# Performance work log

Measured on AMD Instinct MI355X. Metric: run time of the kernel, lower is better.

Reference implementation:

```python
import jax, jax.numpy as jnp
import numpy as np

TEMPERATURE = 8.0  # sqrt(d_k), d_k = 64

def setup_inputs() -> dict:
    key = jax.random.key(0)
    kq, kk, kv, km = jax.random.split(key, 4)
    B, H, S, D = 4, 16, 1024, 64
    q = jax.random.normal(kq, (B, H, S, D), dtype=jnp.float32)
    k = jax.random.normal(kk, (B, H, S, D), dtype=jnp.float32)
    v = jax.random.normal(kv, (B, H, S, D), dtype=jnp.float32)
    mask = jax.random.randint(km, (B, 1, S, S), 0, 2, dtype=jnp.int32)
    return {"q": q, "k": k, "v": v, "mask": mask}

def reference(q, k, v, mask):
    # scores: [B,H,S,S]
    attn = jnp.einsum("bhqd,bhkd->bhqk", q, k) / TEMPERATURE
    attn = jnp.where(mask == 0, jnp.float32(-1e9), attn)
    attn = jax.nn.softmax(attn, axis=-1)
    output = jnp.einsum("bhqk,bhkd->bhqd", attn, v)
    return (output, attn)
```

## Files before the change

kernel.cpp:

```cpp
#include <hip/hip_runtime.h>
#include <hip/hip_bf16.h>

#define S_LEN 1024
#define DH 64
#define QB 64
#define KT 64
#define NKT 16
#define LDP 72

typedef __attribute__((ext_vector_type(8))) short bf16x8;
typedef __attribute__((ext_vector_type(4))) float f32x4;
typedef unsigned long long u64;

__device__ __forceinline__ unsigned short f2bf(float f) {
  unsigned u = __float_as_uint(f);
  u = u + 0x7FFFu + ((u >> 16) & 1u);
  return (unsigned short)(u >> 16);
}
__device__ __forceinline__ float bf2f(unsigned short s) {
  return __uint_as_float((unsigned)s << 16);
}
__device__ __forceinline__ unsigned pk2(float a, float b) {
  __hip_bfloat162 h = __float22bfloat162_rn(float2{a, b});
  return *reinterpret_cast<unsigned*>(&h);
}

__global__ __launch_bounds__(256)
void maskpack_kernel(const int* __restrict__ mask, u64* __restrict__ bits) {
  int w    = blockIdx.x * 4 + (threadIdx.x >> 6);
  int lane = threadIdx.x & 63;
  int m = mask[(size_t)w * 64 + lane];
  u64 word = __ballot(m != 0);
  if (lane == 0) bits[w] = word;
}

__global__ __launch_bounds__(256, 4)
void sdpa_kernel(const float* __restrict__ qg, const float* __restrict__ kg,
                 const float* __restrict__ vg, const u64* __restrict__ bitsg,
                 float* __restrict__ outg, float* __restrict__ attng)
{
  __shared__ unsigned short QsPs[QB][LDP];
  __shared__ unsigned short Ks[KT][LDP];
  __shared__ unsigned short Vt[DH][LDP];
  __shared__ float invLds[QB];

  unsigned short (*Qs)[LDP] = QsPs;
  unsigned short (*Ps)[16][LDP] = (unsigned short (*)[16][LDP])QsPs;

  const int tid  = threadIdx.x;
  const int wid  = tid >> 6;
  const int lane = tid & 63;
  const int lrow = lane & 15;
  const int lhi  = lane >> 4;

  const int P = blockIdx.x;
  const int L = (P & 7) * 128 + (P >> 3);
  const int qbi = L & 15;
  const int bh  = L >> 4;
  const int b   = bh >> 4;

  const size_t qkv_off = (size_t)bh * (S_LEN * DH);
  const float* qb_ptr = qg + qkv_off + (size_t)qbi * QB * DH;
  const float* kb_ptr = kg + qkv_off;
  const float* vb_ptr = vg + qkv_off;
  const int q0 = qbi * QB;
  const int qrow_l = wid * 16 + lhi * 4;

  const u64* bptr = bitsg + ((size_t)(b * S_LEN + q0 + qrow_l)) * NKT;
  float* attn_base = attng + (size_t)bh * (S_LEN * S_LEN);

  float4 Kp[4];
  u64 Bc[4], Bn[4];
  #pragma unroll
  for (int i = 0; i < 4; ++i) {
    int idx = tid + 256 * i;
    Kp[i] = *(const float4*)(kb_ptr + (size_t)(idx >> 4) * DH + ((idx & 15) << 2));
  }
  #pragma unroll
  for (int r = 0; r < 4; ++r) Bc[r] = bptr[r * NKT + 0];

  #pragma unroll
  for (int i = 0; i < 4; ++i) {
    int idx = tid + 256 * i;
    int row = idx >> 4, c4 = (idx & 15) << 2;
    float4 t = *(const float4*)(qb_ptr + row * DH + c4);
    uint2 w; w.x = pk2(t.x, t.y); w.y = pk2(t.z, t.w);
    *(uint2*)&Qs[row][c4] = w;
  }
  __syncthreads();
  const bf16x8 qf0 = *(const bf16x8*)&Qs[wid * 16 + lrow][lhi * 8];
  const bf16x8 qf1 = *(const bf16x8*)&Qs[wid * 16 + lrow][32 + lhi * 8];

  #pragma unroll
  for (int i = 0; i < 4; ++i) {
    int idx = tid + 256 * i;
    int row = idx >> 4, c4 = (idx & 15) << 2;
    float4 t = Kp[i];
    uint2 w; w.x = pk2(t.x, t.y); w.y = pk2(t.z, t.w);
    *(uint2*)&Ks[row][c4] = w;
  }
  #pragma unroll
  for (int i = 0; i < 4; ++i) {
    int idx = tid + 256 * i;
    Kp[i] = *(const float4*)(kb_ptr + (size_t)KT * DH + (size_t)(idx >> 4) * DH + ((idx & 15) << 2));
  }

  float rs[4] = {0.f, 0.f, 0.f, 0.f};

  for (int kt = 0; kt < NKT; ++kt) {
    __syncthreads();

    unsigned short (*cur)[LDP] = (kt & 1) ? Vt : Ks;
    unsigned short (*nxt)[LDP] = (kt & 1) ? Ks : Vt;

    if (kt + 1 < NKT) {
      #pragma unroll
      for (int i = 0; i < 4; ++i) {
        int idx = tid + 256 * i;
        int row = idx >> 4, c4 = (idx & 15) << 2;
        float4 t = Kp[i];
        uint2 w; w.x = pk2(t.x, t.y); w.y = pk2(t.z, t.w);
        *(uint2*)&nxt[row][c4] = w;
      }
      if (kt + 2 < NKT) {
        const float* kn = kb_ptr + (size_t)(kt + 2) * KT * DH;
        #pragma unroll
        for (int i = 0; i < 4; ++i) {
          int idx = tid + 256 * i;
          Kp[i] = *(const float4*)(kn + (size_t)(idx >> 4) * DH + ((idx & 15) << 2));
        }
      }
      #pragma unroll
      for (int r = 0; r < 4; ++r) Bn[r] = bptr[r * NKT + kt + 1];
    }

    #pragma unroll
    for (int nt = 0; nt < 4; ++nt) {
      bf16x8 kf0 = *(const bf16x8*)&cur[nt * 16 + lrow][lhi * 8];
      bf16x8 kf1 = *(const bf16x8*)&cur[nt * 16 + lrow][32 + lhi * 8];
      f32x4 acc = {0.f, 0.f, 0.f, 0.f};
      acc = __builtin_amdgcn_mfma_f32_16x16x32_bf16(qf0, kf0, acc, 0, 0, 0);
      acc = __builtin_amdgcn_mfma_f32_16x16x32_bf16(qf1, kf1, acc, 0, 0, 0);
      #pragma unroll
      for (int r = 0; r < 4; ++r) {
        bool ok = ((Bc[r] >> (nt * 16 + lrow)) & 1ull) != 0;
        float p = ok ? __expf(acc[r] * 0.125f) : 0.f;
        rs[r] += p;
      }
    }
    if (kt + 1 < NKT) {
      #pragma unroll
      for (int r = 0; r < 4; ++r) Bc[r] = Bn[r];
    }
  }

  #pragma unroll
  for (int r = 0; r < 4; ++r) {
    float v = rs[r];
    v += __shfl_xor(v, 1);
    v += __shfl_xor(v, 2);
    v += __shfl_xor(v, 4);
    v += __shfl_xor(v, 8);
    rs[r] = v;
  }
  float inv[4];
  #pragma unroll
  for (int r = 0; r < 4; ++r) inv[r] = 1.0f / rs[r];
  if (lrow == 0) {
    #pragma unroll
    for (int r = 0; r < 4; ++r) invLds[qrow_l + r] = inv[r];
  }

  float4 Vp[4];
  #pragma unroll
  for (int i = 0; i < 4; ++i) {
    int idx = tid + 256 * i;
    Kp[i] = *(const float4*)(kb_ptr + (size_t)(idx >> 4) * DH + ((idx & 15) << 2));
    Vp[i] = *(const float4*)(vb_ptr + (size_t)(idx & 63) * DH + ((idx >> 6) << 2));
  }
  #pragma unroll
  for (int r = 0; r < 4; ++r) Bc[r] = bptr[r * NKT + 0];

  f32x4 oacc[4];
  #pragma unroll
  for (int dt = 0; dt < 4; ++dt) oacc[dt] = (f32x4){0.f, 0.f, 0.f, 0.f};

  for (int kt = 0; kt < NKT; ++kt) {
    __syncthreads();

    #pragma unroll
    for (int i = 0; i < 4; ++i) {
      int idx = tid + 256 * i;
      int row = idx >> 4, c4 = (idx & 15) << 2;
      float4 t = Kp[i];
      uint2 w; w.x = pk2(t.x, t.y); w.y = pk2(t.z, t.w);
      *(uint2*)&Ks[row][c4] = w;
    }
    #pragma unroll
    for (int i = 0; i < 4; ++i) {
      int idx = tid + 256 * i;
      int row = idx & 63, c4 = (idx >> 6) << 2;
      float4 t = Vp[i];
      Vt[c4 + 0][row] = f2bf(t.x);
      Vt[c4 + 1][row] = f2bf(t.y);
      Vt[c4 + 2][row] = f2bf(t.z);
      Vt[c4 + 3][row] = f2bf(t.w);
    }
    if (kt + 1 < NKT) {
      const float* kn = kb_ptr + (size_t)(kt + 1) * KT * DH;
      const float* vn = vb_ptr + (size_t)(kt + 1) * KT * DH;
      #pragma unroll
      for (int i = 0; i < 4; ++i) {
        int idx = tid + 256 * i;
        Kp[i] = *(const float4*)(kn + (size_t)(idx >> 4) * DH + ((idx & 15) << 2));
        Vp[i] = *(const float4*)(vn + (size_t)(idx & 63) * DH + ((idx >> 6) << 2));
      }
      #pragma unroll
      for (int r = 0; r < 4; ++r) Bn[r] = bptr[r * NKT + kt + 1];
    }
    __syncthreads();

    #pragma unroll
    for (int nt = 0; nt < 4; ++nt) {
      bf16x8 kf0 = *(const bf16x8*)&Ks[nt * 16 + lrow][lhi * 8];
      bf16x8 kf1 = *(const bf16x8*)&Ks[nt * 16 + lrow][32 + lhi * 8];
      f32x4 acc = {0.f, 0.f, 0.f, 0.f};
      acc = __builtin_amdgcn_mfma_f32_16x16x32_bf16(qf0, kf0, acc, 0, 0, 0);
      acc = __builtin_amdgcn_mfma_f32_16x16x32_bf16(qf1, kf1, acc, 0, 0, 0);
      #pragma unroll
      for (int r = 0; r < 4; ++r) {
        bool ok = ((Bc[r] >> (nt * 16 + lrow)) & 1ull) != 0;
        float p = ok ? __expf(acc[r] * 0.125f) : 0.f;
        Ps[wid][lhi * 4 + r][nt * 16 + lrow] = f2bf(p);
      }
    }

    asm volatile("" ::: "memory");

    bf16x8 pf0 = *(const bf16x8*)&Ps[wid][lrow][lhi * 8];
    bf16x8 pf1 = *(const bf16x8*)&Ps[wid][lrow][32 + lhi * 8];
    #pragma unroll
    for (int dt = 0; dt < 4; ++dt) {
      bf16x8 vf0 = *(const bf16x8*)&Vt[dt * 16 + lrow][lhi * 8];
      bf16x8 vf1 = *(const bf16x8*)&Vt[dt * 16 + lrow][32 + lhi * 8];
      oacc[dt] = __builtin_amdgcn_mfma_f32_16x16x32_bf16(pf0, vf0, oacc[dt], 0, 0, 0);
      oacc[dt] = __builtin_amdgcn_mfma_f32_16x16x32_bf16(pf1, vf1, oacc[dt], 0, 0, 0);
    }

    {
      float* ab = attn_base + (size_t)(q0 + wid * 16) * S_LEN + kt * KT;
      #pragma unroll
      for (int j = 0; j < 4; ++j) {
        int flat = lane + 64 * j;
        int rowl = flat >> 4;
        int c4   = (flat & 15) << 2;
        float iv = invLds[wid * 16 + rowl];
        const unsigned short* pr = &Ps[wid][rowl][c4];
        f32x4 st;
        st[0] = bf2f(pr[0]) * iv;
        st[1] = bf2f(pr[1]) * iv;
        st[2] = bf2f(pr[2]) * iv;
        st[3] = bf2f(pr[3]) * iv;
        __builtin_nontemporal_store(st, (f32x4*)(ab + (size_t)rowl * S_LEN + c4));
      }
    }

    if (kt + 1 < NKT) {
      #pragma unroll
      for (int r = 0; r < 4; ++r) Bc[r] = Bn[r];
    }
  }

  #pragma unroll
  for (int dt = 0; dt < 4; ++dt)
    #pragma unroll
    for (int r = 0; r < 4; ++r)
      __builtin_nontemporal_store(oacc[dt][r] * inv[r],
          outg + qkv_off + (size_t)(q0 + qrow_l + r) * DH + dt * 16 + lrow);
}

extern "C" void kernel_launch(void* const* d_in, const int* in_sizes, int n_in,
                              void* d_out, int out_size, void* d_ws, size_t ws_size,
                              hipStream_t stream) {
  const float* q    = (const float*)d_in[0];
  const float* k    = (const float*)d_in[1];
  const float* v    = (const float*)d_in[2];
  const int*   mask = (const int*)d_in[3];
  float* out  = (float*)d_out;
  float* attn = out + (size_t)4 * 16 * 1024 * 64;

  const size_t nwords = (size_t)4 * S_LEN * NKT;
  u64* bits = (u64*)d_ws;
  maskpack_kernel<<<dim3(nwords / 4), dim3(256), 0, stream>>>(mask, bits);
  sdpa_kernel<<<dim3(64 * 16), dim3(256), 0, stream>>>(q, k, v, bits, out, attn);
}
```

Before: 110.5 us.

## Double-buffer K and V tiles in LDS to drop one barrier per iteration

Splits the K and V shared-memory tiles into two ping-pong buffers. Each second-pass iteration now writes the next tile into the alternate buffer while computing on the current one, which removes one __syncthreads per iteration and prefetches global loads two tiles ahead. In exchange LDS use roughly doubles for K/V and launch bounds drop to three blocks per CU, which may lower occupancy.

```diff
diff --git a/kernel.cpp b/kernel.cpp
--- a/kernel.cpp
+++ b/kernel.cpp
@@ -34,14 +34,14 @@
   if (lane == 0) bits[w] = word;
 }
 
-__global__ __launch_bounds__(256, 4)
+__global__ __launch_bounds__(256, 3)
 void sdpa_kernel(const float* __restrict__ qg, const float* __restrict__ kg,
                  const float* __restrict__ vg, const u64* __restrict__ bitsg,
                  float* __restrict__ outg, float* __restrict__ attng)
 {
   __shared__ unsigned short QsPs[QB][LDP];
-  __shared__ unsigned short Ks[KT][LDP];
-  __shared__ unsigned short Vt[DH][LDP];
+  __shared__ unsigned short Ksb[2][KT][LDP];
+  __shared__ unsigned short Vtb[2][DH][LDP];
   __shared__ float invLds[QB];
 
   unsigned short (*Qs)[LDP] = QsPs;
@@ -97,7 +97,7 @@
     int row = idx >> 4, c4 = (idx & 15) << 2;
     float4 t = Kp[i];
     uint2 w; w.x = pk2(t.x, t.y); w.y = pk2(t.z, t.w);
-    *(uint2*)&Ks[row][c4] = w;
+    *(uint2*)&Ksb[0][row][c4] = w;
   }
   #pragma unroll
   for (int i = 0; i < 4; ++i) {
@@ -110,8 +110,8 @@
   for (int kt = 0; kt < NKT; ++kt) {
     __syncthreads();
 
-    unsigned short (*cur)[LDP] = (kt & 1) ? Vt : Ks;
-    unsigned short (*nxt)[LDP] = (kt & 1) ? Ks : Vt;
+    unsigned short (*cur)[LDP] = Ksb[kt & 1];
+    unsigned short (*nxt)[LDP] = Ksb[(kt & 1) ^ 1];
 
     if (kt + 1 < NKT) {
       #pragma unroll
@@ -185,45 +185,78 @@
   #pragma unroll
   for (int dt = 0; dt < 4; ++dt) oacc[dt] = (f32x4){0.f, 0.f, 0.f, 0.f};
 
+  __syncthreads();
+  #pragma unroll
+  for (int i = 0; i < 4; ++i) {
+    int idx = tid + 256 * i;
+    int row = idx >> 4, c4 = (idx & 15) << 2;
+    float4 t = Kp[i];
+    uint2 w; w.x = pk2(t.x, t.y); w.y = pk2(t.z, t.w);
+    *(uint2*)&Ksb[0][row][c4] = w;
+  }
+  #pragma unroll
+  for (int i = 0; i < 4; ++i) {
+    int idx = tid + 256 * i;
+    int row = idx & 63, c4 = (idx >> 6) << 2;
+    float4 t = Vp[i];
+    Vtb[0][c4 + 0][row] = f2bf(t.x);
+    Vtb[0][c4 + 1][row] = f2bf(t.y);
+    Vtb[0][c4 + 2][row] = f2bf(t.z);
+    Vtb[0][c4 + 3][row] = f2bf(t.w);
+  }
+  #pragma unroll
+  for (int i = 0; i < 4; ++i) {
+    int idx = tid + 256 * i;
+    Kp[i] = *(const float4*)(kb_ptr + (size_t)KT * DH + (size_t)(idx >> 4) * DH + ((idx & 15) << 2));
+    Vp[i] = *(const float4*)(vb_ptr + (size_t)KT * DH + (size_t)(idx & 63) * DH + ((idx >> 6) << 2));
+  }
+
   for (int kt = 0; kt < NKT; ++kt) {
     __syncthreads();
 
-    #pragma unroll
-    for (int i = 0; i < 4; ++i) {
-      int idx = tid + 256 * i;
-      int row = idx >> 4, c4 = (idx & 15) << 2;
-      float4 t = Kp[i];
-      uint2 w; w.x = pk2(t.x, t.y); w.y = pk2(t.z, t.w);
-      *(uint2*)&Ks[row][c4] = w;
-    }
-    #pragma unroll
-    for (int i = 0; i < 4; ++i) {
-      int idx = tid + 256 * i;
-      int row = idx & 63, c4 = (idx >> 6) << 2;
-      float4 t = Vp[i];
-      Vt[c4 + 0][row] = f2bf(t.x);
-      Vt[c4 + 1][row] = f2bf(t.y);
-      Vt[c4 + 2][row] = f2bf(t.z);
-      Vt[c4 + 3][row] = f2bf(t.w);
-    }
+    const int cb = kt & 1;
+    unsigned short (*Kc)[LDP] = Ksb[cb];
+    unsigned short (*Vc)[LDP] = Vtb[cb];
+
     if (kt + 1 < NKT) {
-      const float* kn = kb_ptr + (size_t)(kt + 1) * KT * DH;
-      const float* vn = vb_ptr + (size_t)(kt + 1) * KT * DH;
+      unsigned short (*Kn)[LDP] = Ksb[cb ^ 1];
+      unsigned short (*Vn)[LDP] = Vtb[cb ^ 1];
       #pragma unroll
       for (int i = 0; i < 4; ++i) {
         int idx = tid + 256 * i;
-        Kp[i] = *(const float4*)(kn + (size_t)(idx >> 4) * DH + ((idx & 15) << 2));
-        Vp[i] = *(const float4*)(vn + (size_t)(idx & 63) * DH + ((idx >> 6) << 2));
+        int row = idx >> 4, c4 = (idx & 15) << 2;
+        float4 t = Kp[i];
+        uint2 w; w.x = pk2(t.x, t.y); w.y = pk2(t.z, t.w);
+        *(uint2*)&Kn[row][c4] = w;
+      }
+      #pragma unroll
+      for (int i = 0; i < 4; ++i) {
+        int idx = tid + 256 * i;
+        int row = idx & 63, c4 = (idx >> 6) << 2;
+        float4 t = Vp[i];
+        Vn[c4 + 0][row] = f2bf(t.x);
+        Vn[c4 + 1][row] = f2bf(t.y);
+        Vn[c4 + 2][row] = f2bf(t.z);
+        Vn[c4 + 3][row] = f2bf(t.w);
+      }
+      if (kt + 2 < NKT) {
+        const float* kn = kb_ptr + (size_t)(kt + 2) * KT * DH;
+        const float* vn = vb_ptr + (size_t)(kt + 2) * KT * DH;
+        #pragma unroll
+        for (int i = 0; i < 4; ++i) {
+          int idx = tid + 256 * i;
+          Kp[i] = *(const float4*)(kn + (size_t)(idx >> 4) * DH + ((idx & 15) << 2));
+          Vp[i] = *(const float4*)(vn + (size_t)(idx & 63) * DH + ((idx >> 6) << 2));
+        }
       }
       #pragma unroll
       for (int r = 0; r < 4; ++r) Bn[r] = bptr[r * NKT + kt + 1];
     }
-    __syncthreads();
 
     #pragma unroll
     for (int nt = 0; nt < 4; ++nt) {
-      bf16x8 kf0 = *(const bf16x8*)&Ks[nt * 16 + lrow][lhi * 8];
-      bf16x8 kf1 = *(const bf16x8*)&Ks[nt * 16 + lrow][32 + lhi * 8];
+      bf16x8 kf0 = *(const bf16x8*)&Kc[nt * 16 + lrow][lhi * 8];
+      bf16x8 kf1 = *(const bf16x8*)&Kc[nt * 16 + lrow][32 + lhi * 8];
       f32x4 acc = {0.f, 0.f, 0.f, 0.f};
       acc = __builtin_amdgcn_mfma_f32_16x16x32_bf16(qf0, kf0, acc, 0, 0, 0);
       acc = __builtin_amdgcn_mfma_f32_16x16x32_bf16(qf1, kf1, acc, 0, 0, 0);
@@ -241,8 +274,8 @@
     bf16x8 pf1 = *(const bf16x8*)&Ps[wid][lrow][32 + lhi * 8];
     #pragma unroll
     for (int dt = 0; dt < 4; ++dt) {
-      bf16x8 vf0 = *(const bf16x8*)&Vt[dt * 16 + lrow][lhi * 8];
-      bf16x8 vf1 = *(const bf16x8*)&Vt[dt * 16 + lrow][32 + lhi * 8];
+      bf16x8 vf0 = *(const bf16x8*)&Vc[dt * 16 + lrow][lhi * 8];
+      bf16x8 vf1 = *(const bf16x8*)&Vc[dt * 16 + lrow][32 + lhi * 8];
       oacc[dt] = __builtin_amdgcn_mfma_f32_16x16x32_bf16(pf0, vf0, oacc[dt], 0, 0, 0);
       oacc[dt] = __builtin_amdgcn_mfma_f32_16x16x32_bf16(pf1, vf1, oacc[dt], 0, 0, 0);
     }
```

New measurement: 108.7 us. Within noise of the previous version (-1.7%).
